# Performance work log

Measured on AMD Instinct MI355X. Metric: run time of the kernel, lower is better.

Reference implementation:

```python
import jax, jax.numpy as jnp
import numpy as np

B, SQ, HIDDEN = 2, 2048, 2048
HEADS, GROUPS, KVC = 16, 4, 128
HPG = HEADS // GROUPS          # heads per group
LAYER_INDEX = 1
SCALE = KVC ** -0.5            # attention_softmax_scale_power = 0.5


def setup_inputs() -> dict:
    key = jax.random.key(0)
    k1, k2, k3, k4 = jax.random.split(key, 4)
    return {
        "x": jax.random.normal(k1, (B, SQ, HIDDEN), jnp.float32),
        "w_q": jax.random.normal(k2, (HIDDEN, HEADS * KVC), jnp.float32) * 0.02,
        "w_kv": jax.random.normal(k3, (HIDDEN, 2 * GROUPS * KVC), jnp.float32) * 0.02,
        "w_dense": jax.random.normal(k4, (HEADS * KVC, HIDDEN), jnp.float32) * 0.02,
    }


def reference(x, w_q, w_kv, w_dense):
    b, sq, _ = x.shape
    sk = sq
    # QKV projections
    q = jnp.einsum("bsh,he->bse", x, w_q).reshape(b, sq, GROUPS, HPG, KVC)
    kv = jnp.einsum("bsh,he->bse", x, w_kv)
    k, v = jnp.split(kv, 2, axis=-1)
    k = k.reshape(b, sk, GROUPS, KVC)
    v = v.reshape(b, sk, GROUPS, KVC)
    # scaled QK^T with the per-layer scale trick: alpha = scale/L in input
    # dtype, then cast to fp32 and multiply by L (as in _attn_fused)
    scores = jnp.einsum("bqgpd,bkgd->bgqpk", q, k) * (SCALE / LAYER_INDEX)
    scores = scores.astype(jnp.float32) * LAYER_INDEX
    # causal mask: mask = ~triu(ones, diagonal=1) -> keep where q_idx >= k_idx
    causal = (jnp.arange(sq)[:, None] >= jnp.arange(sk)[None, :])
    scores = jnp.where(causal[None, None, :, None, :], scores, -jnp.inf)
    probs = jax.nn.softmax(scores, axis=-1).astype(x.dtype)
    # dropout p = 0.0 -> no-op
    ctx = jnp.einsum("bgqpk,bkgd->bqgpd", probs, v).reshape(b, sq, HEADS * KVC)
    return jnp.einsum("bse,eh->bsh", ctx, w_dense)
```

## Files before the change

kernel.cpp:

```cpp
#include <hip/hip_runtime.h>
#include <hip/hip_bf16.h>


typedef __attribute__((ext_vector_type(4))) float f32x4;
typedef __attribute__((ext_vector_type(8))) short bf16x8;
typedef __attribute__((ext_vector_type(4))) short bf16x4;

__device__ __forceinline__ unsigned short f2bf(float f) {
    unsigned u = __builtin_bit_cast(unsigned, f);
    unsigned r = u + 0x7fffu + ((u >> 16) & 1u);
    return (unsigned short)(r >> 16);
}

__device__ __forceinline__ unsigned cvtpk_bf16(float lo, float hi) {
    unsigned r;
    asm("v_cvt_pk_bf16_f32 %0, %1, %2" : "=v"(r) : "v"(lo), "v"(hi));
    return r;
}

__device__ __forceinline__ void gl_lds16(const void* g, void* l) {
    __builtin_amdgcn_global_load_lds(
        (const __attribute__((address_space(1))) unsigned int*)g,
        (__attribute__((address_space(3))) unsigned int*)l, 16, 0, 0);
}

__device__ __forceinline__ int xcd_swizzle(int lin, int nwg) {
    return (lin & 7) * (nwg >> 3) + (lin >> 3);
}

__global__ __launch_bounds__(256)
void xcvt_kernel(const float* __restrict__ in, unsigned short* __restrict__ out)
{
    size_t i = ((size_t)blockIdx.x * 256 + threadIdx.x) * 8;
    float4 a = *reinterpret_cast<const float4*>(&in[i]);
    float4 b = *reinterpret_cast<const float4*>(&in[i + 4]);
    bf16x8 o = { (short)f2bf(a.x), (short)f2bf(a.y),
                 (short)f2bf(a.z), (short)f2bf(a.w),
                 (short)f2bf(b.x), (short)f2bf(b.y),
                 (short)f2bf(b.z), (short)f2bf(b.w) };
    *reinterpret_cast<bf16x8*>(&out[i]) = o;
}

__global__ __launch_bounds__(256)
void wtrans_kernel(const float* __restrict__ in, unsigned short* __restrict__ out,
                   int K, int N)
{
    __shared__ unsigned short T[64][72];
    const int n0 = blockIdx.x * 64, k0 = blockIdx.y * 64;
    const int tid = threadIdx.x;
#pragma unroll
    for (int i = 0; i < 4; ++i) {
        int f = tid + i * 256;
        int r = f >> 4;
        int c4 = (f & 15) * 4;
        float4 v = *reinterpret_cast<const float4*>(&in[(size_t)(k0 + r) * N + n0 + c4]);
        bf16x4 pk = { (short)f2bf(v.x), (short)f2bf(v.y),
                      (short)f2bf(v.z), (short)f2bf(v.w) };
        *reinterpret_cast<bf16x4*>(&T[r][c4]) = pk;
    }
    __syncthreads();
#pragma unroll
    for (int i = 0; i < 2; ++i) {
        int f = tid + i * 256;
        int nn = f >> 3;
        int s8 = (f & 7) * 8;
        bf16x8 o;
#pragma unroll
        for (int j = 0; j < 8; ++j) o[j] = T[s8 + j][nn];
        *reinterpret_cast<bf16x8*>(&out[(size_t)(n0 + nn) * K + k0 + s8]) = o;
    }
}

__global__ __launch_bounds__(256)
void gemm_qkv_kernel(const unsigned short* __restrict__ A,
                     const unsigned short* __restrict__ BT,
                     void* __restrict__ C0v, void* __restrict__ C1v,
                     int M, int N, int K)
{
    __shared__ __align__(16) unsigned short Alds[3][128 * 32];
    __shared__ __align__(16) unsigned short Blds[3][128 * 32];

    const int tid = threadIdx.x;
    const int lane = tid & 63;
    const int wid = tid >> 6;
    const int wr = wid >> 1, wc = wid & 1;
    const int nbx = gridDim.x;
    const int lin = blockIdx.y * nbx + blockIdx.x;
    const int sl = xcd_swizzle(lin, nbx * gridDim.y);
    const int m0 = (sl / nbx) * 128;
    const int n0 = (sl % nbx) * 128;
    const int l16 = lane & 15, lg = lane >> 4;

    f32x4 acc[4][4];
#pragma unroll
    for (int m = 0; m < 4; ++m)
#pragma unroll
        for (int n = 0; n < 4; ++n) acc[m][n] = (f32x4){0.f, 0.f, 0.f, 0.f};

    int srow[2], skb[2];
#pragma unroll
    for (int i = 0; i < 2; ++i) {
        int L = i * 4096 + tid * 16;
        int R = L >> 7, c = L & 127;
        int cp = c ^ ((R & 7) << 4);
        srow[i] = 2 * R + (cp >> 6);
        skb[i]  = cp & 63;
    }

    auto stage = [&](int kt, int bi) {
#pragma unroll
        for (int i = 0; i < 2; ++i) {
            int L = i * 4096 + tid * 16;
            gl_lds16((const char*)A + ((size_t)(m0 + srow[i]) * K + kt) * 2 + skb[i],
                     (char*)(&Alds[bi][0]) + L);
            gl_lds16((const char*)BT + ((size_t)(n0 + srow[i]) * K + kt) * 2 + skb[i],
                     (char*)(&Blds[bi][0]) + L);
        }
    };

    const int NK = K / 32;
    stage(0, 0);
    stage(32, 1);

    for (int t = 0; t < NK; ++t) {
        const int bi = t % 3;
        if (t + 2 < NK) {
            stage((t + 2) * 32, (t + 2) % 3);
            asm volatile("s_waitcnt vmcnt(8)" ::: "memory");
        } else if (t + 1 < NK) {
            asm volatile("s_waitcnt vmcnt(4)" ::: "memory");
        } else {
            asm volatile("s_waitcnt vmcnt(0)" ::: "memory");
        }
        __builtin_amdgcn_s_barrier();

        const char* Ab = (const char*)(&Alds[bi][0]);
        const char* Bb = (const char*)(&Blds[bi][0]);

        bf16x8 af[4], bf[4];
#pragma unroll
        for (int m = 0; m < 4; ++m) {
            int row = wr * 64 + m * 16 + l16;
            int byte = (row >> 1) * 128 +
                       ((((row & 1) << 6) + lg * 16) ^ (((row >> 1) & 7) << 4));
            af[m] = *reinterpret_cast<const bf16x8*>(Ab + byte);
        }
#pragma unroll
        for (int n = 0; n < 4; ++n) {
            int row = wc * 64 + n * 16 + l16;
            int byte = (row >> 1) * 128 +
                       ((((row & 1) << 6) + lg * 16) ^ (((row >> 1) & 7) << 4));
            bf[n] = *reinterpret_cast<const bf16x8*>(Bb + byte);
        }
#pragma unroll
        for (int m = 0; m < 4; ++m)
#pragma unroll
            for (int n = 0; n < 4; ++n)
                acc[m][n] = __builtin_amdgcn_mfma_f32_16x16x32_bf16(
                    af[m], bf[n], acc[m][n], 0, 0, 0);

        __builtin_amdgcn_s_barrier();
    }

#pragma unroll
    for (int m = 0; m < 4; ++m) {
#pragma unroll
        for (int n = 0; n < 4; ++n) {
#pragma unroll
            for (int r = 0; r < 4; ++r) {
                int row = m0 + wr * 64 + m * 16 + lg * 4 + r;
                int col = n0 + wc * 64 + n * 16 + l16;
                float val = acc[m][n][r];
                if (n0 < 2048)
                    ((unsigned short*)C0v)[(size_t)row * 2048 + col] =
                        f2bf(val * 0.12751879523209208f);
                else
                    ((unsigned short*)C1v)[(size_t)row * 1024 + (col - 2048)] = f2bf(val);
            }
        }
    }
}

__global__ __launch_bounds__(256)
void gemm_dense_kernel(const unsigned short* __restrict__ A,
                       const unsigned short* __restrict__ BT,
                       float* __restrict__ C, int M, int N, int K)
{
    __shared__ __align__(16) unsigned short Alds[2][128 * 64];
    __shared__ __align__(16) unsigned short Blds[2][128 * 64];

    const int tid = threadIdx.x;
    const int lane = tid & 63;
    const int wid = tid >> 6;
    const int wr = wid >> 1, wc = wid & 1;
    const int nbx = gridDim.x;
    const int lin = blockIdx.y * nbx + blockIdx.x;
    const int sl = xcd_swizzle(lin, nbx * gridDim.y);
    const int m0 = (sl / nbx) * 128;
    const int n0 = (sl % nbx) * 128;
    const int l16 = lane & 15, lg = lane >> 4;

    f32x4 acc[4][4];
#pragma unroll
    for (int m = 0; m < 4; ++m)
#pragma unroll
        for (int n = 0; n < 4; ++n) acc[m][n] = (f32x4){0.f, 0.f, 0.f, 0.f};

    auto stage = [&](int kt, int bi) {
#pragma unroll
        for (int i = 0; i < 4; ++i) {
            int row = i * 32 + (tid >> 3);
            int cb = ((tid & 7) * 16) ^ ((row & 7) << 4);
            gl_lds16((const char*)A + ((size_t)(m0 + row) * K + kt) * 2 + cb,
                     (char*)(&Alds[bi][0]) + i * 4096 + wid * 1024);
            gl_lds16((const char*)BT + ((size_t)(n0 + row) * K + kt) * 2 + cb,
                     (char*)(&Blds[bi][0]) + i * 4096 + wid * 1024);
        }
    };

    const int NK = K / 64;
    stage(0, 0);
    int cur = 0;

    for (int kti = 0; kti < NK; ++kti) {
        if (kti + 1 < NK) {
            stage((kti + 1) * 64, cur ^ 1);
            asm volatile("s_waitcnt vmcnt(8)" ::: "memory");
        } else {
            asm volatile("s_waitcnt vmcnt(0)" ::: "memory");
        }
        __builtin_amdgcn_s_barrier();

        const char* Ab = (const char*)(&Alds[cur][0]);
        const char* Bb = (const char*)(&Blds[cur][0]);

        bf16x8 af[2][4], bf[2][4];
#pragma unroll
        for (int kd = 0; kd < 2; ++kd) {
#pragma unroll
            for (int m = 0; m < 4; ++m) {
                int row = wr * 64 + m * 16 + l16;
                af[kd][m] = *reinterpret_cast<const bf16x8*>(
                    Ab + row * 128 + ((kd * 64 + lg * 16) ^ ((row & 7) << 4)));
            }
#pragma unroll
            for (int n = 0; n < 4; ++n) {
                int row = wc * 64 + n * 16 + l16;
                bf[kd][n] = *reinterpret_cast<const bf16x8*>(
                    Bb + row * 128 + ((kd * 64 + lg * 16) ^ ((row & 7) << 4)));
            }
        }
#pragma unroll
        for (int kd = 0; kd < 2; ++kd)
#pragma unroll
            for (int m = 0; m < 4; ++m)
#pragma unroll
                for (int n = 0; n < 4; ++n)
                    acc[m][n] = __builtin_amdgcn_mfma_f32_16x16x32_bf16(
                        af[kd][m], bf[kd][n], acc[m][n], 0, 0, 0);

        __builtin_amdgcn_s_barrier();
        cur ^= 1;
    }

#pragma unroll
    for (int m = 0; m < 4; ++m) {
#pragma unroll
        for (int n = 0; n < 4; ++n) {
#pragma unroll
            for (int r = 0; r < 4; ++r) {
                int row = m0 + wr * 64 + m * 16 + lg * 4 + r;
                int col = n0 + wc * 64 + n * 16 + l16;
                C[(size_t)row * N + col] = acc[m][n][r];
            }
        }
    }
}

__global__ __launch_bounds__(256)
void vtrans_kernel(const unsigned short* __restrict__ kv,
                   unsigned short* __restrict__ vt)
{
    __shared__ unsigned short T[64][140];
    const int bg = blockIdx.y;
    const int b = bg >> 2, g = bg & 3;
    const int s0 = blockIdx.x * 64;
    const int tid = threadIdx.x;

#pragma unroll
    for (int i = 0; i < 4; ++i) {
        int f = tid + i * 256;
        int sl = f >> 4;
        int d0 = (f & 15) * 8;
        bf16x8 v = *reinterpret_cast<const bf16x8*>(
            &kv[(size_t)(b * 2048 + s0 + sl) * 1024 + 512 + g * 128 + d0]);
        bf16x4 lo = { v[0], v[1], v[2], v[3] };
        bf16x4 hi = { v[4], v[5], v[6], v[7] };
        *reinterpret_cast<bf16x4*>(&T[sl][d0])     = lo;
        *reinterpret_cast<bf16x4*>(&T[sl][d0 + 4]) = hi;
    }
    __syncthreads();
#pragma unroll
    for (int i = 0; i < 4; ++i) {
        int f = tid + i * 256;
        int d = f >> 3;
        int s8 = (f & 7) * 8;
        bf16x8 o;
#pragma unroll
        for (int j = 0; j < 8; ++j) o[j] = T[s8 + j][d];
        *reinterpret_cast<bf16x8*>(
            &vt[(size_t)(bg * 128 + d) * 2048 + s0 + s8]) = o;
    }
}

__global__ __launch_bounds__(256)
void attn_kernel(const unsigned short* __restrict__ Q,
                 const unsigned short* __restrict__ KV,
                 const unsigned short* __restrict__ VT,
                 unsigned short* __restrict__ CTX)
{
    constexpr int SQ = 2048;
    __shared__ __align__(16) unsigned short Klds[2][64 * 128];
    __shared__ __align__(16) unsigned short Vlds[2][128 * 64];
    __shared__ __align__(16) unsigned short Pl[4][16][64];

    const int tid = threadIdx.x;
    const int lane = tid & 63;
    const int w = tid >> 6;
    const int l16 = lane & 15, lg = lane >> 4;

    const int bid = blockIdx.x;
    const int gb = bid & 7;
    const int g = gb & 3, b = gb >> 2;
    const int pi = bid >> 3;
    const int hh = g * 4 + w;

    const size_t qbase = (size_t)b * SQ * 2048;
    const char* KVb = (const char*)KV + (size_t)b * SQ * 2048;
    const char* VTb = (const char*)VT;

    const int pswz = (l16 & 7) << 3;

    auto stage = [&](int t, int bi) {
        const int k0 = t * 64;
#pragma unroll
        for (int i = 0; i < 4; ++i) {
            int row = w * 16 + i * 4 + (lane >> 4);
            int scol = ((lane & 15) * 16) ^ ((row & 7) << 4);
            gl_lds16(KVb + (size_t)(k0 + row) * 2048 + g * 256 + scol,
                     (char*)(&Klds[bi][0]) + w * 4096 + i * 1024);
        }
#pragma unroll
        for (int i = 0; i < 4; ++i) {
            int row = w * 32 + i * 8 + (lane >> 3);
            int scol = ((lane & 7) * 16) ^ ((row & 7) << 4);
            gl_lds16(VTb + ((size_t)(gb * 128 + row) * 2048 + k0) * 2 + scol,
                     (char*)(&Vlds[bi][0]) + w * 4096 + i * 1024);
        }
    };

#pragma unroll 1
    for (int seg = 0; seg < 2; ++seg) {
        const int qt = seg ? pi : (127 - pi);
        const int ntiles = qt / 4 + 1;

        bf16x8 qfrag[4];
#pragma unroll
        for (int kd = 0; kd < 4; ++kd)
            qfrag[kd] = *reinterpret_cast<const bf16x8*>(
                &Q[qbase + (size_t)(qt * 16 + l16) * 2048 + hh * 128 + kd * 32 + lg * 8]);

        float lsum = 0.f;
        f32x4 acc[8];
#pragma unroll
        for (int nd = 0; nd < 8; ++nd) acc[nd] = (f32x4){0.f,0.f,0.f,0.f};

        stage(0, 0);

        for (int t = 0; t < ntiles; ++t) {
            const int bi = t & 1;
            const int k0 = t * 64;
            if (t + 1 < ntiles) {
                stage(t + 1, bi ^ 1);
                asm volatile("s_waitcnt vmcnt(8)" ::: "memory");
            } else {
                asm volatile("s_waitcnt vmcnt(0)" ::: "memory");
            }
            __builtin_amdgcn_s_barrier();

            const char* Kb = (const char*)(&Klds[bi][0]);
            const char* Vb = (const char*)(&Vlds[bi][0]);

            f32x4 st[4];
#pragma unroll
            for (int nf = 0; nf < 4; ++nf) st[nf] = (f32x4){0.f,0.f,0.f,0.f};
            __builtin_amdgcn_s_setprio(1);
#pragma unroll
            for (int nf = 0; nf < 4; ++nf) {
                int row = nf * 16 + l16;
#pragma unroll
                for (int kd = 0; kd < 4; ++kd) {
                    bf16x8 kf = *reinterpret_cast<const bf16x8*>(
                        Kb + row * 256 + ((kd * 64 + lg * 16) ^ ((row & 7) << 4)));
                    st[nf] = __builtin_amdgcn_mfma_f32_16x16x32_bf16(
                        kf, qfrag[kd], st[nf], 0, 0, 0);
                }
            }
            __builtin_amdgcn_s_setprio(0);

            const bool diag = (t == ntiles - 1);
            {
                float lacc = 0.f;
                const int q = qt * 16 + l16;
#pragma unroll
                for (int nf = 0; nf < 4; ++nf) {
                    float cs0 = st[nf][0];
                    float cs1 = st[nf][1];
                    float cs2 = st[nf][2];
                    float cs3 = st[nf][3];
                    if (diag) {
                        const int keyb = k0 + nf * 16 + lg * 4;
                        if (keyb + 0 > q) cs0 = -INFINITY;
                        if (keyb + 1 > q) cs1 = -INFINITY;
                        if (keyb + 2 > q) cs2 = -INFINITY;
                        if (keyb + 3 > q) cs3 = -INFINITY;
                    }
                    float p0 = exp2f(cs0), p1 = exp2f(cs1);
                    float p2 = exp2f(cs2), p3 = exp2f(cs3);
                    lacc += (p0 + p1) + (p2 + p3);
                    uint2 pk = { cvtpk_bf16(p0, p1), cvtpk_bf16(p2, p3) };
                    *reinterpret_cast<uint2*>(
                        &Pl[w][l16][(nf * 16 + lg * 4) ^ pswz]) = pk;
                }
                lacc += __shfl_xor(lacc, 16, 64);
                lacc += __shfl_xor(lacc, 32, 64);
                lsum += lacc;
            }

            __builtin_amdgcn_s_setprio(1);
#pragma unroll
            for (int kc = 0; kc < 2; ++kc) {
                bf16x8 pf = *reinterpret_cast<const bf16x8*>(
                    &Pl[w][l16][(kc * 32 + lg * 8) ^ pswz]);
#pragma unroll
                for (int nd = 0; nd < 8; ++nd) {
                    int row = nd * 16 + l16;
                    bf16x8 vf = *reinterpret_cast<const bf16x8*>(
                        Vb + row * 128 + ((kc * 64 + lg * 16) ^ ((row & 7) << 4)));
                    acc[nd] = __builtin_amdgcn_mfma_f32_16x16x32_bf16(
                        vf, pf, acc[nd], 0, 0, 0);
                }
            }
            __builtin_amdgcn_s_setprio(0);
            __builtin_amdgcn_s_barrier();
        }

        {
            float inv = 1.0f / lsum;
            const int q = qt * 16 + l16;
#pragma unroll
            for (int nd = 0; nd < 8; ++nd) {
                bf16x4 o = { (short)f2bf(acc[nd][0] * inv),
                             (short)f2bf(acc[nd][1] * inv),
                             (short)f2bf(acc[nd][2] * inv),
                             (short)f2bf(acc[nd][3] * inv) };
                *reinterpret_cast<bf16x4*>(
                    &CTX[qbase + (size_t)q * 2048 + hh * 128 + nd * 16 + lg * 4]) = o;
            }
        }
    }
}

extern "C" void kernel_launch(void* const* d_in, const int* in_sizes, int n_in,
                              void* d_out, int out_size, void* d_ws, size_t ws_size,
                              hipStream_t stream)
{
    const float* x       = (const float*)d_in[0];
    const float* w_q     = (const float*)d_in[1];
    const float* w_kv    = (const float*)d_in[2];
    const float* w_dense = (const float*)d_in[3];

    const int M = 4096;

    char* ws = (char*)d_ws;
    unsigned short* kv_buf  = (unsigned short*)(ws);
    unsigned short* ctx_buf = (unsigned short*)(ws + (8u << 20));
    unsigned short* wqT     = (unsigned short*)(ws + (24u << 20));
    unsigned short* wkvT    = (unsigned short*)(ws + (32u << 20));
    unsigned short* wdT     = wqT;
    unsigned short* xbf    = (unsigned short*)d_out;
    unsigned short* q_buf  = (unsigned short*)d_out + (size_t)M * 2048;
    unsigned short* vt_buf = (unsigned short*)d_out;

    dim3 blk(256);
    xcvt_kernel<<<dim3(4096), blk, 0, stream>>>(x, xbf);
    wtrans_kernel<<<dim3(32, 32), blk, 0, stream>>>(w_q, wqT, 2048, 2048);
    wtrans_kernel<<<dim3(16, 32), blk, 0, stream>>>(w_kv, wkvT, 2048, 1024);
    gemm_qkv_kernel<<<dim3(24, 32), blk, 0, stream>>>(
        xbf, wqT, (void*)q_buf, (void*)kv_buf, M, 3072, 2048);
    wtrans_kernel<<<dim3(32, 32), blk, 0, stream>>>(w_dense, wdT, 2048, 2048);
    vtrans_kernel<<<dim3(32, 8), blk, 0, stream>>>(kv_buf, vt_buf);
    attn_kernel<<<dim3(512), blk, 0, stream>>>(q_buf, kv_buf, vt_buf, ctx_buf);
    gemm_dense_kernel<<<dim3(16, 32), blk, 0, stream>>>(
        ctx_buf, wdT, (float*)d_out, M, 2048, 2048);
}
```

Baseline: 189.3 us.

## Split attention into one q-tile per block with 32-key tiles and more blocks

The attention kernel now launches 1024 blocks, each handling a single 16-row query tile, instead of 512 blocks that each processed a paired short and long tile. Key tiles shrink from 64 to 32, which halves the LDS footprint, and launch bounds request 4 blocks per CU to raise occupancy. A zigzag mapping from block id to query tile is meant to balance causal work across blocks. In exchange there are twice as many barriers and loop iterations per key, and K/V tiles are loaded by more blocks in total.

```diff
diff --git a/kernel.cpp b/kernel.cpp
--- a/kernel.cpp
+++ b/kernel.cpp
@@ -313,16 +313,16 @@
     }
 }
 
-__global__ __launch_bounds__(256)
+__global__ __launch_bounds__(256, 4)
 void attn_kernel(const unsigned short* __restrict__ Q,
                  const unsigned short* __restrict__ KV,
                  const unsigned short* __restrict__ VT,
                  unsigned short* __restrict__ CTX)
 {
     constexpr int SQ = 2048;
-    __shared__ __align__(16) unsigned short Klds[2][64 * 128];
-    __shared__ __align__(16) unsigned short Vlds[2][128 * 64];
-    __shared__ __align__(16) unsigned short Pl[4][16][64];
+    __shared__ __align__(16) unsigned short Klds[2][32 * 128];
+    __shared__ __align__(16) unsigned short Vlds[2][128 * 32];
+    __shared__ __align__(16) unsigned short Pl[4][16][32];
 
     const int tid = threadIdx.x;
     const int lane = tid & 63;
@@ -332,141 +332,140 @@
     const int bid = blockIdx.x;
     const int gb = bid & 7;
     const int g = gb & 3, b = gb >> 2;
-    const int pi = bid >> 3;
+    const int j = bid >> 3;
+    const int qt = (j < 32) ? j : (j < 64) ? (95 - j) : (j < 96) ? j : (223 - j);
+    const int ntiles = qt / 2 + 1;
     const int hh = g * 4 + w;
 
     const size_t qbase = (size_t)b * SQ * 2048;
     const char* KVb = (const char*)KV + (size_t)b * SQ * 2048;
     const char* VTb = (const char*)VT;
 
-    const int pswz = (l16 & 7) << 3;
+    const int pswz = (l16 & 3) << 3;
 
     auto stage = [&](int t, int bi) {
-        const int k0 = t * 64;
-#pragma unroll
-        for (int i = 0; i < 4; ++i) {
-            int row = w * 16 + i * 4 + (lane >> 4);
-            int scol = ((lane & 15) * 16) ^ ((row & 7) << 4);
+        const int k0 = t * 32;
+#pragma unroll
+        for (int i = 0; i < 2; ++i) {
+            int s = i * 256 + tid;
+            int row = s >> 4;
+            int off = (s & 15) * 16;
+            int scol = off ^ ((row & 7) << 4);
             gl_lds16(KVb + (size_t)(k0 + row) * 2048 + g * 256 + scol,
-                     (char*)(&Klds[bi][0]) + w * 4096 + i * 1024);
-        }
-#pragma unroll
-        for (int i = 0; i < 4; ++i) {
-            int row = w * 32 + i * 8 + (lane >> 3);
-            int scol = ((lane & 7) * 16) ^ ((row & 7) << 4);
+                     (char*)(&Klds[bi][0]) + s * 16);
+        }
+#pragma unroll
+        for (int i = 0; i < 2; ++i) {
+            int s = i * 256 + tid;
+            int row = s >> 2;
+            int off = (s & 3) * 16;
+            int scol = off ^ ((row & 3) << 4);
             gl_lds16(VTb + ((size_t)(gb * 128 + row) * 2048 + k0) * 2 + scol,
-                     (char*)(&Vlds[bi][0]) + w * 4096 + i * 1024);
+                     (char*)(&Vlds[bi][0]) + s * 16);
         }
     };
 
-#pragma unroll 1
-    for (int seg = 0; seg < 2; ++seg) {
-        const int qt = seg ? pi : (127 - pi);
-        const int ntiles = qt / 4 + 1;
-
-        bf16x8 qfrag[4];
-#pragma unroll
-        for (int kd = 0; kd < 4; ++kd)
-            qfrag[kd] = *reinterpret_cast<const bf16x8*>(
-                &Q[qbase + (size_t)(qt * 16 + l16) * 2048 + hh * 128 + kd * 32 + lg * 8]);
-
-        float lsum = 0.f;
-        f32x4 acc[8];
-#pragma unroll
-        for (int nd = 0; nd < 8; ++nd) acc[nd] = (f32x4){0.f,0.f,0.f,0.f};
-
-        stage(0, 0);
-
-        for (int t = 0; t < ntiles; ++t) {
-            const int bi = t & 1;
-            const int k0 = t * 64;
-            if (t + 1 < ntiles) {
-                stage(t + 1, bi ^ 1);
-                asm volatile("s_waitcnt vmcnt(8)" ::: "memory");
-            } else {
-                asm volatile("s_waitcnt vmcnt(0)" ::: "memory");
-            }
-            __builtin_amdgcn_s_barrier();
-
-            const char* Kb = (const char*)(&Klds[bi][0]);
-            const char* Vb = (const char*)(&Vlds[bi][0]);
-
-            f32x4 st[4];
-#pragma unroll
-            for (int nf = 0; nf < 4; ++nf) st[nf] = (f32x4){0.f,0.f,0.f,0.f};
-            __builtin_amdgcn_s_setprio(1);
-#pragma unroll
-            for (int nf = 0; nf < 4; ++nf) {
-                int row = nf * 16 + l16;
-#pragma unroll
-                for (int kd = 0; kd < 4; ++kd) {
-                    bf16x8 kf = *reinterpret_cast<const bf16x8*>(
-                        Kb + row * 256 + ((kd * 64 + lg * 16) ^ ((row & 7) << 4)));
-                    st[nf] = __builtin_amdgcn_mfma_f32_16x16x32_bf16(
-                        kf, qfrag[kd], st[nf], 0, 0, 0);
+    bf16x8 qfrag[4];
+#pragma unroll
+    for (int kd = 0; kd < 4; ++kd)
+        qfrag[kd] = *reinterpret_cast<const bf16x8*>(
+            &Q[qbase + (size_t)(qt * 16 + l16) * 2048 + hh * 128 + kd * 32 + lg * 8]);
+
+    float lsum = 0.f;
+    f32x4 acc[8];
+#pragma unroll
+    for (int nd = 0; nd < 8; ++nd) acc[nd] = (f32x4){0.f,0.f,0.f,0.f};
+
+    stage(0, 0);
+
+    for (int t = 0; t < ntiles; ++t) {
+        const int bi = t & 1;
+        const int k0 = t * 32;
+        if (t + 1 < ntiles) {
+            stage(t + 1, bi ^ 1);
+            asm volatile("s_waitcnt vmcnt(4)" ::: "memory");
+        } else {
+            asm volatile("s_waitcnt vmcnt(0)" ::: "memory");
+        }
+        __builtin_amdgcn_s_barrier();
+
+        const char* Kb = (const char*)(&Klds[bi][0]);
+        const char* Vb = (const char*)(&Vlds[bi][0]);
+
+        f32x4 st[2];
+        st[0] = (f32x4){0.f,0.f,0.f,0.f};
+        st[1] = (f32x4){0.f,0.f,0.f,0.f};
+        __builtin_amdgcn_s_setprio(1);
+#pragma unroll
+        for (int nf = 0; nf < 2; ++nf) {
+            int row = nf * 16 + l16;
+#pragma unroll
+            for (int kd = 0; kd < 4; ++kd) {
+                bf16x8 kf = *reinterpret_cast<const bf16x8*>(
+                    Kb + row * 256 + ((kd * 64 + lg * 16) ^ ((row & 7) << 4)));
+                st[nf] = __builtin_amdgcn_mfma_f32_16x16x32_bf16(
+                    kf, qfrag[kd], st[nf], 0, 0, 0);
+            }
+        }
+        __builtin_amdgcn_s_setprio(0);
+
+        const bool diag = (t == ntiles - 1);
+        {
+            float lacc = 0.f;
+            const int q = qt * 16 + l16;
+#pragma unroll
+            for (int nf = 0; nf < 2; ++nf) {
+                float cs0 = st[nf][0];
+                float cs1 = st[nf][1];
+                float cs2 = st[nf][2];
+                float cs3 = st[nf][3];
+                if (diag) {
+                    const int keyb = k0 + nf * 16 + lg * 4;
+                    if (keyb + 0 > q) cs0 = -INFINITY;
+                    if (keyb + 1 > q) cs1 = -INFINITY;
+                    if (keyb + 2 > q) cs2 = -INFINITY;
+                    if (keyb + 3 > q) cs3 = -INFINITY;
                 }
-            }
-            __builtin_amdgcn_s_setprio(0);
-
-            const bool diag = (t == ntiles - 1);
-            {
-                float lacc = 0.f;
-                const int q = qt * 16 + l16;
-#pragma unroll
-                for (int nf = 0; nf < 4; ++nf) {
-                    float cs0 = st[nf][0];
-                    float cs1 = st[nf][1];
-                    float cs2 = st[nf][2];
-                    float cs3 = st[nf][3];
-                    if (diag) {
-                        const int keyb = k0 + nf * 16 + lg * 4;
-                        if (keyb + 0 > q) cs0 = -INFINITY;
-                        if (keyb + 1 > q) cs1 = -INFINITY;
-                        if (keyb + 2 > q) cs2 = -INFINITY;
-                        if (keyb + 3 > q) cs3 = -INFINITY;
-                    }
-                    float p0 = exp2f(cs0), p1 = exp2f(cs1);
-                    float p2 = exp2f(cs2), p3 = exp2f(cs3);
-                    lacc += (p0 + p1) + (p2 + p3);
-                    uint2 pk = { cvtpk_bf16(p0, p1), cvtpk_bf16(p2, p3) };
-                    *reinterpret_cast<uint2*>(
-                        &Pl[w][l16][(nf * 16 + lg * 4) ^ pswz]) = pk;
-                }
-                lacc += __shfl_xor(lacc, 16, 64);
-                lacc += __shfl_xor(lacc, 32, 64);
-                lsum += lacc;
-            }
-
-            __builtin_amdgcn_s_setprio(1);
-#pragma unroll
-            for (int kc = 0; kc < 2; ++kc) {
-                bf16x8 pf = *reinterpret_cast<const bf16x8*>(
-                    &Pl[w][l16][(kc * 32 + lg * 8) ^ pswz]);
-#pragma unroll
-                for (int nd = 0; nd < 8; ++nd) {
-                    int row = nd * 16 + l16;
-                    bf16x8 vf = *reinterpret_cast<const bf16x8*>(
-                        Vb + row * 128 + ((kc * 64 + lg * 16) ^ ((row & 7) << 4)));
-                    acc[nd] = __builtin_amdgcn_mfma_f32_16x16x32_bf16(
-                        vf, pf, acc[nd], 0, 0, 0);
-                }
-            }
-            __builtin_amdgcn_s_setprio(0);
-            __builtin_amdgcn_s_barrier();
-        }
-
+                float p0 = exp2f(cs0), p1 = exp2f(cs1);
+                float p2 = exp2f(cs2), p3 = exp2f(cs3);
+                lacc += (p0 + p1) + (p2 + p3);
+                uint2 pk = { cvtpk_bf16(p0, p1), cvtpk_bf16(p2, p3) };
+                *reinterpret_cast<uint2*>(
+                    &Pl[w][l16][(nf * 16 + lg * 4) ^ pswz]) = pk;
+            }
+            lacc += __shfl_xor(lacc, 16, 64);
+            lacc += __shfl_xor(lacc, 32, 64);
+            lsum += lacc;
+        }
+
+        __builtin_amdgcn_s_setprio(1);
         {
-            float inv = 1.0f / lsum;
-            const int q = qt * 16 + l16;
+            bf16x8 pf = *reinterpret_cast<const bf16x8*>(
+                &Pl[w][l16][(lg * 8) ^ pswz]);
 #pragma unroll
             for (int nd = 0; nd < 8; ++nd) {
-                bf16x4 o = { (short)f2bf(acc[nd][0] * inv),
-                             (short)f2bf(acc[nd][1] * inv),
-                             (short)f2bf(acc[nd][2] * inv),
-                             (short)f2bf(acc[nd][3] * inv) };
-                *reinterpret_cast<bf16x4*>(
-                    &CTX[qbase + (size_t)q * 2048 + hh * 128 + nd * 16 + lg * 4]) = o;
-            }
+                int row = nd * 16 + l16;
+                bf16x8 vf = *reinterpret_cast<const bf16x8*>(
+                    Vb + row * 64 + ((lg * 16) ^ ((row & 3) << 4)));
+                acc[nd] = __builtin_amdgcn_mfma_f32_16x16x32_bf16(
+                    vf, pf, acc[nd], 0, 0, 0);
+            }
+        }
+        __builtin_amdgcn_s_setprio(0);
+        __builtin_amdgcn_s_barrier();
+    }
+
+    {
+        float inv = 1.0f / lsum;
+        const int q = qt * 16 + l16;
+#pragma unroll
+        for (int nd = 0; nd < 8; ++nd) {
+            bf16x4 o = { (short)f2bf(acc[nd][0] * inv),
+                         (short)f2bf(acc[nd][1] * inv),
+                         (short)f2bf(acc[nd][2] * inv),
+                         (short)f2bf(acc[nd][3] * inv) };
+            *reinterpret_cast<bf16x4*>(
+                &CTX[qbase + (size_t)q * 2048 + hh * 128 + nd * 16 + lg * 4]) = o;
         }
     }
 }
@@ -500,7 +499,7 @@
         xbf, wqT, (void*)q_buf, (void*)kv_buf, M, 3072, 2048);
     wtrans_kernel<<<dim3(32, 32), blk, 0, stream>>>(w_dense, wdT, 2048, 2048);
     vtrans_kernel<<<dim3(32, 8), blk, 0, stream>>>(kv_buf, vt_buf);
-    attn_kernel<<<dim3(512), blk, 0, stream>>>(q_buf, kv_buf, vt_buf, ctx_buf);
+    attn_kernel<<<dim3(1024), blk, 0, stream>>>(q_buf, kv_buf, vt_buf, ctx_buf);
     gemm_dense_kernel<<<dim3(16, 32), blk, 0, stream>>>(
         ctx_buf, wdT, (float*)d_out, M, 2048, 2048);
 }
```

Result: slower. 203.6 us (+7.6%).
